# Kernel tuning notes

Measured on AMD Instinct MI355X. Metric: run time of the kernel, lower is better.

Reference implementation:

```python
import jax, jax.numpy as jnp
import numpy as np

N_FILTERS = 1024
N_HEADS = 8  # hardcoded h=8 in the original einops.rearrange
LN_EPS = 1e-3  # keras LayerNormalization default epsilon


def setup_inputs() -> dict:
    key = jax.random.key(0)
    k1, k2, k3 = jax.random.split(key, 3)
    B, N, C = 4, 2048, N_FILTERS
    x = jax.random.normal(k1, (B, N, C), dtype=jnp.float32)
    ln_gamma = jnp.ones((C,), dtype=jnp.float32)
    ln_beta = jnp.zeros((C,), dtype=jnp.float32)
    w_qkv = jax.random.normal(k2, (C, 3 * C), dtype=jnp.float32) * 0.02
    w_out = jax.random.normal(k3, (C, C), dtype=jnp.float32) * 0.02
    b_out = jnp.zeros((C,), dtype=jnp.float32)
    return {"x": x, "ln_gamma": ln_gamma, "ln_beta": ln_beta,
            "w_qkv": w_qkv, "w_out": w_out, "b_out": b_out}


def reference(x, ln_gamma, ln_beta, w_qkv, w_out, b_out):
    B, N, C = x.shape
    h = N_HEADS
    hd = C // h
    scale = jnp.asarray(float(C) ** (-0.5), dtype=x.dtype)  # note: full C, as in source

    # LayerNorm over last axis (keras default)
    mu = jnp.mean(x, axis=-1, keepdims=True)
    var = jnp.var(x, axis=-1, keepdims=True)
    xn = (x - mu) / jnp.sqrt(var + LN_EPS) * ln_gamma + ln_beta

    # QKV projection (no bias): [B, N, 3C]
    qkv = jnp.einsum('bnc,cd->bnd', xn, w_qkv)
    # rearrange 'b n (qkv h c) -> qkv b h n c'
    qkv = qkv.reshape(B, N, 3, h, hd).transpose(2, 0, 3, 1, 4)
    q, k, v = qkv[0], qkv[1], qkv[2]

    # attention: [B, h, N, N]
    scores = jnp.einsum('bhnc,bhmc->bhnm', q, k) * scale
    attn = jax.nn.softmax(scores, axis=-1)
    out = jnp.einsum('bhnm,bhmc->bhnc', attn, v)
    # 'b h n c -> b n (h c)'
    out = out.transpose(0, 2, 1, 3).reshape(B, N, C)

    out = jnp.einsum('bnc,cd->bnd', out, w_out) + b_out
    return x + out
```

## Files before the change

### kernel.cpp

```cpp
#include <hip/hip_runtime.h>

typedef _Float16 half8 __attribute__((ext_vector_type(8)));
typedef float floatx4 __attribute__((ext_vector_type(4)));

#define BB 4
#define SEQ 2048
#define CHN 1024
#define NH 8
#define HD 128
#define CQ 3072

__device__ __forceinline__ float bf2f(unsigned short b) {
  unsigned int u = ((unsigned int)b) << 16;
  float f; __builtin_memcpy(&f, &u, 4); return f;
}
__device__ __forceinline__ unsigned short f2bf(float f) {
  unsigned int u; __builtin_memcpy(&u, &f, 4);
  u += 0x7fffu + ((u >> 16) & 1u);
  return (unsigned short)(u >> 16);
}
__device__ __forceinline__ void gl_lds16(const _Float16* g, _Float16* l) {
  __builtin_amdgcn_global_load_lds(
      (const __attribute__((address_space(1))) unsigned int*)(g),
      (__attribute__((address_space(3))) unsigned int*)(l), 16, 0, 0);
}

__global__ __launch_bounds__(256) void detect_k(
    const unsigned int* __restrict__ x, int* __restrict__ flag) {
  __shared__ int bad;
  if (threadIdx.x == 0) bad = 0;
  __syncthreads();
  int b = 0;
#pragma unroll
  for (int i = 0; i < 8; ++i) {
    unsigned int w = x[threadIdx.x * 8 + i];
    float v = bf2f((unsigned short)(w & 0xffffu));
    if (!(fabsf(v) < 1e4f)) b = 1;
  }
  if (b) bad = 1;
  __syncthreads();
  if (threadIdx.x == 0) *flag = bad;
}

__global__ __launch_bounds__(256) void transpose_b2h(
    const void* __restrict__ in, _Float16* __restrict__ out, int R, int C,
    const int* __restrict__ flag) {
  __shared__ _Float16 tile[64][66];
  int isf = *flag;
  int ti = blockIdx.y, tj = blockIdx.x, t = threadIdx.x;
  if (isf) {
    const float* inf = (const float*)in;
#pragma unroll
    for (int i = 0; i < 16; ++i) {
      int lin = i * 256 + t;
      int r = lin >> 6, c = lin & 63;
      tile[r][c] = (_Float16)inf[(size_t)(ti * 64 + r) * C + tj * 64 + c];
    }
  } else {
    const unsigned short* inb = (const unsigned short*)in;
#pragma unroll
    for (int i = 0; i < 16; ++i) {
      int lin = i * 256 + t;
      int r = lin >> 6, c = lin & 63;
      tile[r][c] = (_Float16)bf2f(inb[(size_t)(ti * 64 + r) * C + tj * 64 + c]);
    }
  }
  __syncthreads();
#pragma unroll
  for (int i = 0; i < 16; ++i) {
    int lin = i * 256 + t;
    int c = lin >> 6, r = lin & 63;
    out[(size_t)(tj * 64 + c) * R + ti * 64 + r] = tile[r][c];
  }
}

__global__ __launch_bounds__(256) void ln_k(
    const void* __restrict__ xv, const void* __restrict__ gv,
    const void* __restrict__ bv, _Float16* __restrict__ xn,
    const int* __restrict__ flag) {
  int isf = *flag;
  int row = blockIdx.x, t = threadIdx.x;
  float v0, v1, v2, v3;
  if (isf) {
    const float4 f = *reinterpret_cast<const float4*>((const float*)xv + (size_t)row * CHN + t * 4);
    v0 = f.x; v1 = f.y; v2 = f.z; v3 = f.w;
  } else {
    ushort4 u = *reinterpret_cast<const ushort4*>((const unsigned short*)xv + (size_t)row * CHN + t * 4);
    v0 = bf2f(u.x); v1 = bf2f(u.y); v2 = bf2f(u.z); v3 = bf2f(u.w);
  }
  float s = v0 + v1 + v2 + v3;
  float ss = v0 * v0 + v1 * v1 + v2 * v2 + v3 * v3;
#pragma unroll
  for (int off = 32; off >= 1; off >>= 1) {
    s += __shfl_xor(s, off, 64);
    ss += __shfl_xor(ss, off, 64);
  }
  __shared__ float red[8];
  int wave = t >> 6, lane = t & 63;
  if (lane == 0) { red[wave] = s; red[4 + wave] = ss; }
  __syncthreads();
  s = red[0] + red[1] + red[2] + red[3];
  ss = red[4] + red[5] + red[6] + red[7];
  float mu = s * (1.0f / CHN);
  float var = ss * (1.0f / CHN) - mu * mu;
  float rstd = rsqrtf(var + 1e-3f);
  float g0, g1, g2, g3, b0, b1, b2, b3;
  if (isf) {
    const float4 g = *reinterpret_cast<const float4*>((const float*)gv + t * 4);
    const float4 b = *reinterpret_cast<const float4*>((const float*)bv + t * 4);
    g0 = g.x; g1 = g.y; g2 = g.z; g3 = g.w;
    b0 = b.x; b1 = b.y; b2 = b.z; b3 = b.w;
  } else {
    ushort4 g = *reinterpret_cast<const ushort4*>((const unsigned short*)gv + t * 4);
    ushort4 b = *reinterpret_cast<const ushort4*>((const unsigned short*)bv + t * 4);
    g0 = bf2f(g.x); g1 = bf2f(g.y); g2 = bf2f(g.z); g3 = bf2f(g.w);
    b0 = bf2f(b.x); b1 = bf2f(b.y); b2 = bf2f(b.z); b3 = bf2f(b.w);
  }
  _Float16* o = xn + (size_t)row * CHN + t * 4;
  o[0] = (_Float16)((v0 - mu) * rstd * g0 + b0);
  o[1] = (_Float16)((v1 - mu) * rstd * g1 + b1);
  o[2] = (_Float16)((v2 - mu) * rstd * g2 + b2);
  o[3] = (_Float16)((v3 - mu) * rstd * g3 + b3);
}

template <int EPI>
__global__ __launch_bounds__(256, 3) void gemm_k(
    const _Float16* __restrict__ A, const _Float16* __restrict__ Bt,
    int M, int Nn, int K,
    _Float16* __restrict__ outh, void* __restrict__ outv,
    const void* __restrict__ bias, const void* __restrict__ resid,
    const int* __restrict__ flag) {
  __shared__ _Float16 As[128 * 64];
  __shared__ _Float16 Bs[128 * 64];
  int isf = (EPI == 1) ? *flag : 0;
  int t = threadIdx.x;
  int wave = t >> 6, lane = t & 63, quad = lane >> 4, l15 = lane & 15;
  int wm = wave >> 1, wn = wave & 1;
  size_t arow0 = (size_t)blockIdx.y * 128;
  size_t brow0 = (size_t)blockIdx.x * 128;
  int lr = lane >> 3, lc = lane & 7;
  int gc = lc ^ lr;
  const _Float16* Abase = A + (arow0 + wave * 32 + lr) * (size_t)K + gc * 8;
  const _Float16* Bbase = Bt + (brow0 + wave * 32 + lr) * (size_t)K + gc * 8;
  floatx4 acc[4][4] = {};
  int nkt = K >> 6;
  for (int kt = 0; kt < nkt; ++kt) {
#pragma unroll
    for (int i = 0; i < 4; ++i) {
      gl_lds16(Abase + kt * 64 + (size_t)i * 8 * K, As + (wave * 32 + i * 8) * 64);
      gl_lds16(Bbase + kt * 64 + (size_t)i * 8 * K, Bs + (wave * 32 + i * 8) * 64);
    }
    __syncthreads();
#pragma unroll
    for (int ks = 0; ks < 2; ++ks) {
      half8 af[4], bfr[4];
#pragma unroll
      for (int mt = 0; mt < 4; ++mt) {
        int row = wm * 64 + mt * 16 + l15;
        int slot = (ks * 4 + quad) ^ (l15 & 7);
        af[mt] = *reinterpret_cast<const half8*>(As + row * 64 + slot * 8);
      }
#pragma unroll
      for (int nt = 0; nt < 4; ++nt) {
        int row = wn * 64 + nt * 16 + l15;
        int slot = (ks * 4 + quad) ^ (l15 & 7);
        bfr[nt] = *reinterpret_cast<const half8*>(Bs + row * 64 + slot * 8);
      }
#pragma unroll
      for (int mt = 0; mt < 4; ++mt)
#pragma unroll
        for (int nt = 0; nt < 4; ++nt)
          acc[mt][nt] = __builtin_amdgcn_mfma_f32_16x16x32_f16(af[mt], bfr[nt], acc[mt][nt], 0, 0, 0);
    }
    __syncthreads();
  }
#pragma unroll
  for (int mt = 0; mt < 4; ++mt) {
#pragma unroll
    for (int r = 0; r < 4; ++r) {
      size_t row = arow0 + wm * 64 + mt * 16 + quad * 4 + r;
#pragma unroll
      for (int nt = 0; nt < 4; ++nt) {
        size_t col = brow0 + wn * 64 + nt * 16 + l15;
        float v = acc[mt][nt][r];
        if (EPI == 0) {
          outh[row * Nn + col] = (_Float16)v;
        } else {
          if (isf) {
            v += ((const float*)bias)[col] + ((const float*)resid)[row * Nn + col];
            ((float*)outv)[row * Nn + col] = v;
          } else {
            v += bf2f(((const unsigned short*)bias)[col]) +
                 bf2f(((const unsigned short*)resid)[row * Nn + col]);
            ((unsigned short*)outv)[row * Nn + col] = f2bf(v);
          }
        }
      }
    }
  }
}

__global__ __launch_bounds__(256) void vtrans_k(
    const _Float16* __restrict__ qkv, _Float16* __restrict__ vtr) {
  __shared__ _Float16 tile[64][72];
  int t = threadIdx.x;
  int tok0 = blockIdx.x * 64;
  int hd0 = blockIdx.y * 64;
  int bh = blockIdx.z;
  int b = bh >> 3, h = bh & 7;
  const _Float16* src = qkv + (size_t)b * SEQ * CQ + 2 * CHN + h * HD + hd0;
#pragma unroll
  for (int i = 0; i < 2; ++i) {
    int lin = i * 256 + t;
    int r = lin >> 3, c8 = lin & 7;
    *reinterpret_cast<half8*>(&tile[r][c8 * 8]) =
        *reinterpret_cast<const half8*>(src + (size_t)(tok0 + r) * CQ + c8 * 8);
  }
  __syncthreads();
  _Float16* dst = vtr + ((size_t)bh * HD + hd0) * SEQ + tok0;
#pragma unroll
  for (int i = 0; i < 2; ++i) {
    int lin = i * 256 + t;
    int c = lin >> 3, r8 = lin & 7;
    half8 v;
#pragma unroll
    for (int j = 0; j < 8; ++j) v[j] = tile[r8 * 8 + j][c];
    *reinterpret_cast<half8*>(dst + (size_t)c * SEQ + r8 * 8) = v;
  }
}

__global__ __launch_bounds__(256, 2) void attn_k(
    const _Float16* __restrict__ qkv, const _Float16* __restrict__ vtr,
    _Float16* __restrict__ out) {
  __shared__ _Float16 Ks[2][64 * 128];
  __shared__ _Float16 Vs[128 * 64];
  __shared__ _Float16 pl[4 * 32 * 64];
  int t = threadIdx.x;
  int wave = t >> 6, lane = t & 63, quad = lane >> 4, l15 = lane & 15;
  int bh = blockIdx.x & 31;
  int qt = blockIdx.x >> 5;
  int b = bh >> 3, h = bh & 7;
  int qbase = qt * 128;
  const _Float16* qp = qkv + (size_t)b * SEQ * CQ + h * HD;
  const _Float16* kp = qp + CHN;
  const _Float16* vtp = vtr + (size_t)bh * HD * SEQ;
  const _Float16 qsc = (_Float16)0.045085299f;
  half8 aq[2][4];
#pragma unroll
  for (int qs = 0; qs < 2; ++qs) {
    const _Float16* qr = qp + (size_t)(qbase + wave * 32 + qs * 16 + l15) * CQ + quad * 8;
#pragma unroll
    for (int c = 0; c < 4; ++c) {
      half8 v = *reinterpret_cast<const half8*>(qr + c * 32);
#pragma unroll
      for (int j = 0; j < 8; ++j) v[j] = v[j] * qsc;
      aq[qs][c] = v;
    }
  }
  float l_p[2][4] = {};
  floatx4 accO[2][8] = {};
  _Float16* pw = pl + wave * (32 * 64);
  int kr = lane >> 4, ks16 = lane & 15;
  int vr = lane >> 3, vs8 = lane & 7;
#pragma unroll
  for (int i = 0; i < 4; ++i) {
    int r = wave * 16 + i * 4 + kr;
    int gcs = ks16 ^ (r & 15);
    gl_lds16(kp + (size_t)r * CQ + gcs * 8, Ks[0] + (wave * 16 + i * 4) * 128);
  }
  __syncthreads();
  for (int kt = 0; kt < SEQ / 64; ++kt) {
    int kb = kt * 64;
#pragma unroll
    for (int i = 0; i < 4; ++i) {
      int r = wave * 32 + i * 8 + vr;
      int gcs = vs8 ^ (r & 7);
      gl_lds16(vtp + (size_t)r * SEQ + kb + gcs * 8, Vs + (wave * 32 + i * 8) * 64);
    }
    if (kt + 1 < SEQ / 64) {
      const _Float16* kn = kp + (size_t)(kb + 64) * CQ;
      _Float16* kdst = Ks[(kt + 1) & 1];
#pragma unroll
      for (int i = 0; i < 4; ++i) {
        int r = wave * 16 + i * 4 + kr;
        int gcs = ks16 ^ (r & 15);
        gl_lds16(kn + (size_t)r * CQ + gcs * 8, kdst + (wave * 16 + i * 4) * 128);
      }
    }
    const _Float16* kc = Ks[kt & 1];
    floatx4 accS[2][4] = {};
#pragma unroll
    for (int c = 0; c < 4; ++c)
#pragma unroll
      for (int nt = 0; nt < 4; ++nt) {
        int row = nt * 16 + l15;
        half8 bk = *reinterpret_cast<const half8*>(kc + (row * 16 + ((c * 4 + quad) ^ l15)) * 8);
        accS[0][nt] = __builtin_amdgcn_mfma_f32_16x16x32_f16(aq[0][c], bk, accS[0][nt], 0, 0, 0);
        accS[1][nt] = __builtin_amdgcn_mfma_f32_16x16x32_f16(aq[1][c], bk, accS[1][nt], 0, 0, 0);
      }
#pragma unroll
    for (int qs = 0; qs < 2; ++qs)
#pragma unroll
      for (int nt = 0; nt < 4; ++nt)
#pragma unroll
        for (int r = 0; r < 4; ++r) {
          float p = __builtin_amdgcn_exp2f(accS[qs][nt][r]);
          l_p[qs][r] += p;
          int prow = qs * 16 + quad * 4 + r;
          int pcol = nt * 16 + l15;
          pw[prow * 64 + ((((pcol >> 3) ^ (prow & 7)) << 3) | (pcol & 7))] = (_Float16)p;
        }
    __syncthreads();
#pragma unroll
    for (int c2 = 0; c2 < 2; ++c2) {
      int pslot = (c2 * 4 + quad) ^ (l15 & 7);
      half8 ap0 = *reinterpret_cast<const half8*>(pw + l15 * 64 + pslot * 8);
      half8 ap1 = *reinterpret_cast<const half8*>(pw + (16 + l15) * 64 + pslot * 8);
#pragma unroll
      for (int o = 0; o < 8; ++o) {
        int row = o * 16 + l15;
        half8 bv = *reinterpret_cast<const half8*>(Vs + (row * 8 + ((c2 * 4 + quad) ^ (l15 & 7))) * 8);
        accO[0][o] = __builtin_amdgcn_mfma_f32_16x16x32_f16(ap0, bv, accO[0][o], 0, 0, 0);
        accO[1][o] = __builtin_amdgcn_mfma_f32_16x16x32_f16(ap1, bv, accO[1][o], 0, 0, 0);
      }
    }
    __syncthreads();
  }
#pragma unroll
  for (int qs = 0; qs < 2; ++qs)
#pragma unroll
    for (int r = 0; r < 4; ++r) {
      float l = l_p[qs][r];
#pragma unroll
      for (int off = 8; off >= 1; off >>= 1) l += __shfl_xor(l, off, 64);
      float inv = 1.0f / l;
      size_t row = qbase + wave * 32 + qs * 16 + quad * 4 + r;
      _Float16* orow = out + ((size_t)b * SEQ + row) * CHN + h * HD;
#pragma unroll
      for (int o = 0; o < 8; ++o) orow[o * 16 + l15] = (_Float16)(accO[qs][o][r] * inv);
    }
}

extern "C" void kernel_launch(void* const* d_in, const int* in_sizes, int n_in,
                              void* d_out, int out_size, void* d_ws, size_t ws_size,
                              hipStream_t stream) {
  (void)in_sizes; (void)n_in; (void)out_size; (void)ws_size;
  const void* x = d_in[0];
  const void* gam = d_in[1];
  const void* bet = d_in[2];
  const void* wqkv = d_in[3];
  const void* wout = d_in[4];
  const void* bout = d_in[5];
  char* ws = (char*)d_ws;
  _Float16* xn    = (_Float16*)(ws);
  _Float16* vtr   = (_Float16*)(ws);
  _Float16* qkv   = (_Float16*)(ws + (size_t)16777216);
  _Float16* aout  = (_Float16*)(ws + (size_t)67108864);
  _Float16* wqkvT = (_Float16*)(ws + (size_t)83886080);
  _Float16* woutT = (_Float16*)(ws + (size_t)90177536);
  int* flag       = (int*)(ws + (size_t)92274688);

  detect_k<<<1, 256, 0, stream>>>((const unsigned int*)x, flag);
  transpose_b2h<<<dim3(CQ / 64, CHN / 64), 256, 0, stream>>>(wqkv, wqkvT, CHN, CQ, flag);
  transpose_b2h<<<dim3(CHN / 64, CHN / 64), 256, 0, stream>>>(wout, woutT, CHN, CHN, flag);
  ln_k<<<dim3(BB * SEQ), 256, 0, stream>>>(x, gam, bet, xn, flag);
  gemm_k<0><<<dim3(CQ / 128, BB * SEQ / 128), 256, 0, stream>>>(
      xn, wqkvT, BB * SEQ, CQ, CHN, qkv, nullptr, nullptr, nullptr, flag);
  vtrans_k<<<dim3(SEQ / 64, HD / 64, BB * NH), 256, 0, stream>>>(qkv, vtr);
  attn_k<<<dim3(BB * NH * (SEQ / 128)), 256, 0, stream>>>(qkv, vtr, aout);
  gemm_k<1><<<dim3(CHN / 128, BB * SEQ / 128), 256, 0, stream>>>(
      aout, woutT, BB * SEQ, CHN, CHN, nullptr, d_out, bout, x, flag);
}
```

Measured before the change: 287.9 us.

## Fuse V transpose into QKV GEMM epilogue and stage outputs through LDS

The QKV GEMM epilogue now writes its accumulator tile into shared memory with an XOR swizzle. Blocks covering the V columns store that tile transposed straight into the vtr buffer, which lets the separate vtrans kernel be dropped. All GEMM outputs, including the residual/bias epilogue, are now written as coalesced 16-byte vectors instead of scattered scalar stores. vtr now lives in d_out, which is only safe because the output projection overwrites it after attention has read it. The LayerNorm edit swaps bias b2 for b.w and then reloads it in a second step, an odd change with no speed purpose.

Result: slower. 296.4 us (+2.9%).

```diff
diff --git a/kernel.cpp b/kernel.cpp
--- a/kernel.cpp
+++ b/kernel.cpp
@@ -114,7 +114,11 @@
     ushort4 g = *reinterpret_cast<const ushort4*>((const unsigned short*)gv + t * 4);
     ushort4 b = *reinterpret_cast<const ushort4*>((const unsigned short*)bv + t * 4);
     g0 = bf2f(g.x); g1 = bf2f(g.y); g2 = bf2f(g.z); g3 = bf2f(g.w);
-    b0 = bf2f(b.x); b1 = bf2f(b.y); b2 = bf2f(b.z); b3 = bf2f(b.w);
+    b0 = bf2f(b.x); b1 = bf2f(b.y); b2 = bf2f(b.w); b3 = bf2f(b.w);
+  }
+  if (!isf) {
+    ushort4 b = *reinterpret_cast<const ushort4*>((const unsigned short*)bv + t * 4);
+    b2 = bf2f(b.z);
   }
   _Float16* o = xn + (size_t)row * CHN + t * 4;
   o[0] = (_Float16)((v0 - mu) * rstd * g0 + b0);
@@ -127,11 +131,13 @@
 __global__ __launch_bounds__(256, 3) void gemm_k(
     const _Float16* __restrict__ A, const _Float16* __restrict__ Bt,
     int M, int Nn, int K,
-    _Float16* __restrict__ outh, void* __restrict__ outv,
+    _Float16* __restrict__ outh, _Float16* __restrict__ vtr,
+    void* __restrict__ outv,
     const void* __restrict__ bias, const void* __restrict__ resid,
     const int* __restrict__ flag) {
-  __shared__ _Float16 As[128 * 64];
-  __shared__ _Float16 Bs[128 * 64];
+  __shared__ _Float16 smem[128 * 64 * 2];
+  _Float16* As = smem;
+  _Float16* Bs = smem + 128 * 64;
   int isf = (EPI == 1) ? *flag : 0;
   int t = threadIdx.x;
   int wave = t >> 6, lane = t & 63, quad = lane >> 4, l15 = lane & 15;
@@ -174,58 +180,83 @@
     }
     __syncthreads();
   }
-#pragma unroll
-  for (int mt = 0; mt < 4; ++mt) {
+  bool isv = (EPI == 0) && (brow0 >= 2048);
+  _Float16* Cs = smem;
+#pragma unroll
+  for (int mt = 0; mt < 4; ++mt)
 #pragma unroll
     for (int r = 0; r < 4; ++r) {
-      size_t row = arow0 + wm * 64 + mt * 16 + quad * 4 + r;
+      int row = wm * 64 + mt * 16 + quad * 4 + r;
 #pragma unroll
       for (int nt = 0; nt < 4; ++nt) {
-        size_t col = brow0 + wn * 64 + nt * 16 + l15;
-        float v = acc[mt][nt][r];
-        if (EPI == 0) {
-          outh[row * Nn + col] = (_Float16)v;
-        } else {
-          if (isf) {
-            v += ((const float*)bias)[col] + ((const float*)resid)[row * Nn + col];
-            ((float*)outv)[row * Nn + col] = v;
-          } else {
-            v += bf2f(((const unsigned short*)bias)[col]) +
-                 bf2f(((const unsigned short*)resid)[row * Nn + col]);
-            ((unsigned short*)outv)[row * Nn + col] = f2bf(v);
-          }
-        }
-      }
-    }
-  }
-}
-
-__global__ __launch_bounds__(256) void vtrans_k(
-    const _Float16* __restrict__ qkv, _Float16* __restrict__ vtr) {
-  __shared__ _Float16 tile[64][72];
-  int t = threadIdx.x;
-  int tok0 = blockIdx.x * 64;
-  int hd0 = blockIdx.y * 64;
-  int bh = blockIdx.z;
-  int b = bh >> 3, h = bh & 7;
-  const _Float16* src = qkv + (size_t)b * SEQ * CQ + 2 * CHN + h * HD + hd0;
-#pragma unroll
-  for (int i = 0; i < 2; ++i) {
-    int lin = i * 256 + t;
-    int r = lin >> 3, c8 = lin & 7;
-    *reinterpret_cast<half8*>(&tile[r][c8 * 8]) =
-        *reinterpret_cast<const half8*>(src + (size_t)(tok0 + r) * CQ + c8 * 8);
-  }
-  __syncthreads();
-  _Float16* dst = vtr + ((size_t)bh * HD + hd0) * SEQ + tok0;
-#pragma unroll
-  for (int i = 0; i < 2; ++i) {
-    int lin = i * 256 + t;
-    int c = lin >> 3, r8 = lin & 7;
-    half8 v;
-#pragma unroll
-    for (int j = 0; j < 8; ++j) v[j] = tile[r8 * 8 + j][c];
-    *reinterpret_cast<half8*>(dst + (size_t)c * SEQ + r8 * 8) = v;
+        int col = wn * 64 + nt * 16 + l15;
+        _Float16 hv = (_Float16)acc[mt][nt][r];
+        if (isv)
+          Cs[col * 128 + ((((row >> 3) ^ (col & 15)) << 3) | (row & 7))] = hv;
+        else
+          Cs[row * 128 + ((((col >> 3) ^ (row & 15)) << 3) | (col & 7))] = hv;
+      }
+    }
+  __syncthreads();
+  int rr = t >> 4, cc = t & 15;
+  if (EPI == 0) {
+    if (isv) {
+      int bq = (int)(arow0 >> 11), tok0 = (int)(arow0 & 2047);
+      int h = (int)((brow0 - 2048) >> 7);
+      _Float16* vb = vtr + (size_t)(bq * 8 + h) * 128 * SEQ;
+#pragma unroll
+      for (int i = 0; i < 8; ++i) {
+        int vc = i * 16 + rr;
+        half8 v8 = *reinterpret_cast<const half8*>(Cs + vc * 128 + ((cc ^ (vc & 15)) << 3));
+        *reinterpret_cast<half8*>(vb + (size_t)vc * SEQ + tok0 + cc * 8) = v8;
+      }
+    } else {
+#pragma unroll
+      for (int i = 0; i < 8; ++i) {
+        int row = i * 16 + rr;
+        half8 v8 = *reinterpret_cast<const half8*>(Cs + row * 128 + ((cc ^ (row & 15)) << 3));
+        *reinterpret_cast<half8*>(outh + (arow0 + row) * Nn + brow0 + cc * 8) = v8;
+      }
+    }
+  } else {
+#pragma unroll
+    for (int i = 0; i < 8; ++i) {
+      int row = i * 16 + rr;
+      half8 v8 = *reinterpret_cast<const half8*>(Cs + row * 128 + ((cc ^ (row & 15)) << 3));
+      size_t g = (arow0 + row) * (size_t)Nn + brow0 + cc * 8;
+      int cb = (int)brow0 + cc * 8;
+      if (isf) {
+        const float4* rp = reinterpret_cast<const float4*>((const float*)resid + g);
+        const float4* bp = reinterpret_cast<const float4*>((const float*)bias + cb);
+        float4 r0 = rp[0], r1 = rp[1], b0 = bp[0], b1 = bp[1];
+        float4 o0, o1;
+        o0.x = (float)v8[0] + r0.x + b0.x;
+        o0.y = (float)v8[1] + r0.y + b0.y;
+        o0.z = (float)v8[2] + r0.z + b0.z;
+        o0.w = (float)v8[3] + r0.w + b0.w;
+        o1.x = (float)v8[4] + r1.x + b1.x;
+        o1.y = (float)v8[5] + r1.y + b1.y;
+        o1.z = (float)v8[6] + r1.z + b1.z;
+        o1.w = (float)v8[7] + r1.w + b1.w;
+        float4* op = reinterpret_cast<float4*>((float*)outv + g);
+        op[0] = o0; op[1] = o1;
+      } else {
+        const ushort4* rp = reinterpret_cast<const ushort4*>((const unsigned short*)resid + g);
+        const ushort4* bp = reinterpret_cast<const ushort4*>((const unsigned short*)bias + cb);
+        ushort4 r0 = rp[0], r1 = rp[1], b0 = bp[0], b1 = bp[1];
+        ushort4 o0, o1;
+        o0.x = f2bf((float)v8[0] + bf2f(r0.x) + bf2f(b0.x));
+        o0.y = f2bf((float)v8[1] + bf2f(r0.y) + bf2f(b0.y));
+        o0.z = f2bf((float)v8[2] + bf2f(r0.z) + bf2f(b0.z));
+        o0.w = f2bf((float)v8[3] + bf2f(r0.w) + bf2f(b0.w));
+        o1.x = f2bf((float)v8[4] + bf2f(r1.x) + bf2f(b1.x));
+        o1.y = f2bf((float)v8[5] + bf2f(r1.y) + bf2f(b1.y));
+        o1.z = f2bf((float)v8[6] + bf2f(r1.z) + bf2f(b1.z));
+        o1.w = f2bf((float)v8[7] + bf2f(r1.w) + bf2f(b1.w));
+        ushort4* op = reinterpret_cast<ushort4*>((unsigned short*)outv + g);
+        op[0] = o0; op[1] = o1;
+      }
+    }
   }
 }
 
@@ -353,21 +384,20 @@
   const void* bout = d_in[5];
   char* ws = (char*)d_ws;
   _Float16* xn    = (_Float16*)(ws);
-  _Float16* vtr   = (_Float16*)(ws);
   _Float16* qkv   = (_Float16*)(ws + (size_t)16777216);
   _Float16* aout  = (_Float16*)(ws + (size_t)67108864);
   _Float16* wqkvT = (_Float16*)(ws + (size_t)83886080);
   _Float16* woutT = (_Float16*)(ws + (size_t)90177536);
   int* flag       = (int*)(ws + (size_t)92274688);
+  _Float16* vtr   = (_Float16*)d_out;
 
   detect_k<<<1, 256, 0, stream>>>((const unsigned int*)x, flag);
   transpose_b2h<<<dim3(CQ / 64, CHN / 64), 256, 0, stream>>>(wqkv, wqkvT, CHN, CQ, flag);
   transpose_b2h<<<dim3(CHN / 64, CHN / 64), 256, 0, stream>>>(wout, woutT, CHN, CHN, flag);
   ln_k<<<dim3(BB * SEQ), 256, 0, stream>>>(x, gam, bet, xn, flag);
   gemm_k<0><<<dim3(CQ / 128, BB * SEQ / 128), 256, 0, stream>>>(
-      xn, wqkvT, BB * SEQ, CQ, CHN, qkv, nullptr, nullptr, nullptr, flag);
-  vtrans_k<<<dim3(SEQ / 64, HD / 64, BB * NH), 256, 0, stream>>>(qkv, vtr);
+      xn, wqkvT, BB * SEQ, CQ, CHN, qkv, vtr, nullptr, nullptr, nullptr, flag);
   attn_k<<<dim3(BB * NH * (SEQ / 128)), 256, 0, stream>>>(qkv, vtr, aout);
   gemm_k<1><<<dim3(CHN / 128, BB * SEQ / 128), 256, 0, stream>>>(
-      aout, woutT, BB * SEQ, CHN, CHN, nullptr, d_out, bout, x, flag);
-}
+      aout, woutT, BB * SEQ, CHN, CHN, nullptr, nullptr, d_out, bout, x, flag);
+}
```
